# Optimization experiments

Measured on AMD Instinct MI355X. Metric: run time of the kernel, lower is better.

The kernel has to match this reference:

```python
import jax, jax.numpy as jnp
import numpy as np

D_EMB = 256
SCALE = 0.02
B, T = 4, 4096
EPS = 1e-5


def layer_norm(x, w, b):
    m = jnp.mean(x, axis=-1, keepdims=True)
    v = jnp.mean((x - m) ** 2, axis=-1, keepdims=True)
    return (x - m) * jax.lax.rsqrt(v + EPS) * w + b


def setup_inputs() -> dict:
    key = jax.random.key(0)
    ks = jax.random.split(key, 4)
    x = jax.random.normal(ks[0], (B, T, D_EMB), dtype=jnp.float32)
    qkv = jax.random.normal(ks[1], (3, D_EMB, D_EMB), dtype=jnp.float32) * SCALE
    # nn.Linear(D, 2D, bias=False): weight shape (2D, D), applied as x @ W.T
    w1 = jax.random.normal(ks[2], (2 * D_EMB, D_EMB), dtype=jnp.float32) * (1.0 / np.sqrt(D_EMB))
    w2 = jax.random.normal(ks[3], (D_EMB, 2 * D_EMB), dtype=jnp.float32) * (1.0 / np.sqrt(2 * D_EMB))
    ones = jnp.ones((D_EMB,), dtype=jnp.float32)
    zeros = jnp.zeros((D_EMB,), dtype=jnp.float32)
    return {
        "x": x, "qkv": qkv,
        "ln_q_w": ones, "ln_q_b": zeros,
        "ln_k_w": ones, "ln_k_b": zeros,
        "ln_attn_w": ones, "ln_attn_b": zeros,
        "w1": w1, "w2": w2,
        "ln_ff_w": ones, "ln_ff_b": zeros,
    }


def reference(x, qkv, ln_q_w, ln_q_b, ln_k_w, ln_k_b, ln_attn_w, ln_attn_b, w1, w2, ln_ff_w, ln_ff_b):
    # QKV projections: [3, B, T, D]
    y = jnp.einsum('btd,ndD->nbtD', x, qkv)
    q, k, v = y[0], y[1], y[2]
    q = layer_norm(q, ln_q_w, ln_q_b)
    k = layer_norm(k, ln_k_w, ln_k_b)
    # full (non-causal) single-head attention, scale by sqrt(D_EMB)
    scores = jnp.einsum('btd,bsd->bts', q, k) / jnp.sqrt(jnp.float32(D_EMB))
    attn = jax.nn.softmax(scores, axis=-1)
    y = jnp.einsum('bts,bsd->btd', attn, v)
    y = layer_norm(y, ln_attn_w, ln_attn_b)
    x = 0.7 * (x + y)
    # FFN with dual leaky_relu
    y = jax.nn.leaky_relu(x @ w1.T, negative_slope=0.2)
    y = jax.nn.leaky_relu(y @ w2.T, negative_slope=0.2)
    y = layer_norm(y, ln_ff_w, ln_ff_b)
    return 0.7 * (x + y)
```

## Files before the change

### kernel.cpp

```cpp
#include <hip/hip_runtime.h>

#define BSZ   4
#define TSEQ  4096
#define DEMB  256
#define NTOK  (BSZ * TSEQ)
#define HID   512
#define SPLITS 4
#define KEYS_PER_SPLIT (TSEQ / SPLITS)
#define TK 32
#define KIMG_STRIDE 8704
#define VIMG_STRIDE 10240

using bf16x8 = __attribute__((ext_vector_type(8))) short;
using f32x16 = __attribute__((ext_vector_type(16))) float;

static __device__ __forceinline__ unsigned short f2bf(float f) {
  union { float f; unsigned u; } v; v.f = f;
  unsigned r = v.u + 0x7FFF + ((v.u >> 16) & 1);
  return (unsigned short)(r >> 16);
}
static __device__ __forceinline__ float bf2f(unsigned short u) {
  union { unsigned u; float f; } v; v.u = ((unsigned)u) << 16;
  return v.f;
}

static __device__ __forceinline__ void async16(void* lds, const void* gp) {
  __builtin_amdgcn_global_load_lds(
      (const __attribute__((address_space(1))) unsigned int*)gp,
      (__attribute__((address_space(3))) unsigned int*)lds, 16, 0, 0);
}

__global__ __launch_bounds__(256) void qkvT_kernel(
    const float* __restrict__ qkv, unsigned short* __restrict__ qkvT)
{
  __shared__ float Ts[64][65];
  const int tid = threadIdx.x;
  const int k0 = blockIdx.x * 64;
  const int j0 = blockIdx.y * 64;
  const int z  = blockIdx.z;
  const float* src = qkv + (size_t)z * DEMB * DEMB + (size_t)k0 * DEMB + j0;
#pragma unroll
  for (int p = 0; p < 4; ++p) {
    int idx = p * 256 + tid;
    int r = idx >> 4, g = idx & 15;
    float4 v = *(const float4*)(src + (size_t)r * DEMB + g * 4);
    Ts[r][g * 4 + 0] = v.x; Ts[r][g * 4 + 1] = v.y;
    Ts[r][g * 4 + 2] = v.z; Ts[r][g * 4 + 3] = v.w;
  }
  __syncthreads();
  unsigned short* dst = qkvT + (size_t)z * DEMB * DEMB + (size_t)j0 * DEMB + k0;
#pragma unroll
  for (int p = 0; p < 4; ++p) {
    int idx = p * 256 + tid;
    int r = idx >> 4, g = idx & 15;
    ushort4 o;
    o.x = f2bf(Ts[g * 4 + 0][r]); o.y = f2bf(Ts[g * 4 + 1][r]);
    o.z = f2bf(Ts[g * 4 + 2][r]); o.w = f2bf(Ts[g * 4 + 3][r]);
    *(ushort4*)(dst + (size_t)r * DEMB + g * 4) = o;
  }
}

__global__ __launch_bounds__(256) void castw_kernel(
    const float* __restrict__ w1, const float* __restrict__ w2,
    unsigned short* __restrict__ w1b, unsigned short* __restrict__ w2b)
{
  const int i = blockIdx.x * 256 + threadIdx.x;
  const float* s = blockIdx.y ? w2 : w1;
  unsigned short* d = blockIdx.y ? w2b : w1b;
  float4 v = ((const float4*)s)[i];
  ushort4 o;
  o.x = f2bf(v.x); o.y = f2bf(v.y); o.z = f2bf(v.z); o.w = f2bf(v.w);
  ((ushort4*)d)[i] = o;
}

template <int ACT, int MODE, int AF32>
__global__ __launch_bounds__(256, 3) void gemm_bf16_kernel(
    const void* __restrict__ Av, const unsigned short* __restrict__ Bt,
    float* __restrict__ Cf, unsigned short* __restrict__ C0,
    unsigned short* __restrict__ C1, unsigned short* __restrict__ C2,
    int M, int N, int K)
{
  __shared__ __align__(16) unsigned short As[128 * 72];
  __shared__ __align__(16) unsigned short Bs[128 * 72];

  const int tid = threadIdx.x;
  const int w   = tid >> 6;
  const int wm  = w >> 1, wn = w & 1;
  const int l   = tid & 63;
  const int lm  = l & 31;
  const int lh  = l >> 5;

  const int m0    = blockIdx.x * 128;
  const int nbase = blockIdx.y * 128;

  f32x16 acc00, acc01, acc10, acc11;
#pragma unroll
  for (int r = 0; r < 16; ++r) { acc00[r] = 0.f; acc01[r] = 0.f; acc10[r] = 0.f; acc11[r] = 0.f; }

  const int lr = tid >> 3;
  const int lc = (tid & 7) * 8;
  const int fr = tid >> 4;
  const int fc = (tid & 15) * 4;

  const unsigned short* Ab = (const unsigned short*)Av;
  const float* Af = (const float*)Av;

  bf16x8 arb[4], brb[4];
  float4 arf[8];

#pragma unroll
  for (int i = 0; i < (AF32 ? 8 : 4); ++i) {
    if (AF32) arf[i] = *(const float4*)(Af + (size_t)(m0 + i * 16 + fr) * K + fc);
    else      arb[i] = *(const bf16x8*)(Ab + (size_t)(m0 + i * 32 + lr) * K + lc);
  }
#pragma unroll
  for (int i = 0; i < 4; ++i)
    brb[i] = *(const bf16x8*)(Bt + (size_t)(nbase + i * 32 + lr) * K + lc);

  for (int k0 = 0; k0 < K; k0 += 64) {
    __syncthreads();
    if (AF32) {
#pragma unroll
      for (int i = 0; i < 8; ++i) {
        ushort4 u;
        u.x = f2bf(arf[i].x); u.y = f2bf(arf[i].y);
        u.z = f2bf(arf[i].z); u.w = f2bf(arf[i].w);
        *(ushort4*)&As[(i * 16 + fr) * 72 + fc] = u;
      }
    } else {
#pragma unroll
      for (int i = 0; i < 4; ++i) *(bf16x8*)&As[(i * 32 + lr) * 72 + lc] = arb[i];
    }
#pragma unroll
    for (int i = 0; i < 4; ++i) *(bf16x8*)&Bs[(i * 32 + lr) * 72 + lc] = brb[i];
    __syncthreads();

    if (k0 + 64 < K) {
      const int kn = k0 + 64;
#pragma unroll
      for (int i = 0; i < (AF32 ? 8 : 4); ++i) {
        if (AF32) arf[i] = *(const float4*)(Af + (size_t)(m0 + i * 16 + fr) * K + kn + fc);
        else      arb[i] = *(const bf16x8*)(Ab + (size_t)(m0 + i * 32 + lr) * K + kn + lc);
      }
#pragma unroll
      for (int i = 0; i < 4; ++i)
        brb[i] = *(const bf16x8*)(Bt + (size_t)(nbase + i * 32 + lr) * K + kn + lc);
    }

#pragma unroll
    for (int ks = 0; ks < 4; ++ks) {
      bf16x8 a0 = *(const bf16x8*)&As[(wm * 64 + lm)      * 72 + ks * 16 + lh * 8];
      bf16x8 a1 = *(const bf16x8*)&As[(wm * 64 + 32 + lm) * 72 + ks * 16 + lh * 8];
      bf16x8 b0 = *(const bf16x8*)&Bs[(wn * 64 + lm)      * 72 + ks * 16 + lh * 8];
      bf16x8 b1 = *(const bf16x8*)&Bs[(wn * 64 + 32 + lm) * 72 + ks * 16 + lh * 8];
      acc00 = __builtin_amdgcn_mfma_f32_32x32x16_bf16(a0, b0, acc00, 0, 0, 0);
      acc01 = __builtin_amdgcn_mfma_f32_32x32x16_bf16(a0, b1, acc01, 0, 0, 0);
      acc10 = __builtin_amdgcn_mfma_f32_32x32x16_bf16(a1, b0, acc10, 0, 0, 0);
      acc11 = __builtin_amdgcn_mfma_f32_32x32x16_bf16(a1, b1, acc11, 0, 0, 0);
    }
  }

  unsigned short* Cb = C0;
  int col0, ldc;
  if (MODE == 2) {
    const int sel = blockIdx.y >> 1;
    Cb = (sel == 0) ? C0 : (sel == 1 ? C1 : C2);
    col0 = (blockIdx.y & 1) * 128;
    ldc = DEMB;
  } else {
    col0 = nbase;
    ldc = N;
  }
  const f32x16* accs[4] = { &acc00, &acc01, &acc10, &acc11 };
#pragma unroll
  for (int am = 0; am < 2; ++am)
#pragma unroll
    for (int bn = 0; bn < 2; ++bn) {
      const f32x16& a = *accs[am * 2 + bn];
#pragma unroll
      for (int r = 0; r < 16; ++r) {
        const int m = m0 + wm * 64 + am * 32 + (r & 3) + 8 * (r >> 2) + 4 * lh;
        const int n = col0 + wn * 64 + bn * 32 + lm;
        float v = a[r];
        if (ACT == 1) v = v > 0.f ? v : 0.2f * v;
        if (MODE == 0) Cf[(size_t)m * ldc + n] = v;
        else           Cb[(size_t)m * ldc + n] = f2bf(v);
      }
    }
}

template <int IMG>
__global__ __launch_bounds__(256) void ln_bf16b_kernel(
    const unsigned short* __restrict__ X, const float* __restrict__ w,
    const float* __restrict__ b, unsigned short* __restrict__ out)
{
  const int lane = threadIdx.x & 63;
  const size_t row = (size_t)blockIdx.x * 4 + (threadIdx.x >> 6);
  ushort4 u = *(const ushort4*)&X[row * DEMB + lane * 4];
  float x0 = bf2f(u.x), x1 = bf2f(u.y), x2 = bf2f(u.z), x3 = bf2f(u.w);
  float s  = x0 + x1 + x2 + x3;
  float sq = x0 * x0 + x1 * x1 + x2 * x2 + x3 * x3;
#pragma unroll
  for (int o = 32; o > 0; o >>= 1) { s += __shfl_down(s, o); sq += __shfl_down(sq, o); }
  s = __shfl(s, 0); sq = __shfl(sq, 0);
  const float m  = s * (1.f / DEMB);
  const float rs = rsqrtf(sq * (1.f / DEMB) - m * m + 1e-5f);
  const float4 wv = *(const float4*)&w[lane * 4];
  const float4 bv = *(const float4*)&b[lane * 4];
  ushort4 o;
  o.x = f2bf((x0 - m) * rs * wv.x + bv.x);
  o.y = f2bf((x1 - m) * rs * wv.y + bv.y);
  o.z = f2bf((x2 - m) * rs * wv.z + bv.z);
  o.w = f2bf((x3 - m) * rs * wv.w + bv.w);
  if (IMG == 0) {
    *(ushort4*)&out[row * DEMB + lane * 4] = o;
  } else {
    const int bb = (int)(row >> 12);
    const int t  = (int)(row & 4095);
    *(ushort4*)&out[(size_t)(bb * 128 + (t >> 5)) * KIMG_STRIDE + (t & 31) * 264 + lane * 4] = o;
  }
}

__global__ __launch_bounds__(256) void ln_res_kernel(
    const float* __restrict__ Y, const float* __restrict__ Xin,
    const float* __restrict__ w, const float* __restrict__ b,
    float* __restrict__ Out)
{
  const int lane = threadIdx.x & 63;
  const size_t row = (size_t)blockIdx.x * 4 + (threadIdx.x >> 6);
  float4 y = *(const float4*)&Y[row * DEMB + lane * 4];
  float s  = y.x + y.y + y.z + y.w;
  float sq = y.x * y.x + y.y * y.y + y.z * y.z + y.w * y.w;
#pragma unroll
  for (int o = 32; o > 0; o >>= 1) { s += __shfl_down(s, o); sq += __shfl_down(sq, o); }
  s = __shfl(s, 0); sq = __shfl(sq, 0);
  const float m  = s * (1.f / DEMB);
  const float rs = rsqrtf(sq * (1.f / DEMB) - m * m + 1e-5f);
  const float4 wv = *(const float4*)&w[lane * 4];
  const float4 bv = *(const float4*)&b[lane * 4];
  const float4 xi = *(const float4*)&Xin[row * DEMB + lane * 4];
  float4 o;
  o.x = 0.7f * (xi.x + (y.x - m) * rs * wv.x + bv.x);
  o.y = 0.7f * (xi.y + (y.y - m) * rs * wv.y + bv.y);
  o.z = 0.7f * (xi.z + (y.z - m) * rs * wv.z + bv.z);
  o.w = 0.7f * (xi.w + (y.w - m) * rs * wv.w + bv.w);
  *(float4*)&Out[row * DEMB + lane * 4] = o;
}

__global__ __launch_bounds__(256) void vtrans_img_kernel(
    const unsigned short* __restrict__ Vraw, unsigned short* __restrict__ Vimg)
{
  __shared__ float Ts[64][65];
  const int tid = threadIdx.x;
  const int t0 = blockIdx.x * 64;
  const int d0 = blockIdx.y * 64;
  const int b  = blockIdx.z;
  const unsigned short* src = Vraw + ((size_t)b * TSEQ + t0) * DEMB + d0;
#pragma unroll
  for (int p = 0; p < 4; ++p) {
    int idx = p * 256 + tid;
    int r = idx >> 4, g = idx & 15;
    ushort4 u = *(const ushort4*)(src + (size_t)r * DEMB + g * 4);
    Ts[r][g * 4 + 0] = bf2f(u.x); Ts[r][g * 4 + 1] = bf2f(u.y);
    Ts[r][g * 4 + 2] = bf2f(u.z); Ts[r][g * 4 + 3] = bf2f(u.w);
  }
  __syncthreads();
#pragma unroll
  for (int p = 0; p < 4; ++p) {
    int idx = p * 256 + tid;
    int r = idx >> 4, g = idx & 15;
    const int t  = t0 + g * 4;
    const int kt = t >> 5, toff = t & 31;
    ushort4 o;
    o.x = f2bf(Ts[g * 4 + 0][r]); o.y = f2bf(Ts[g * 4 + 1][r]);
    o.z = f2bf(Ts[g * 4 + 2][r]); o.w = f2bf(Ts[g * 4 + 3][r]);
    *(ushort4*)(Vimg + (size_t)(b * 128 + kt) * VIMG_STRIDE + (d0 + r) * 40 + toff) = o;
  }
}

__global__ __launch_bounds__(256, 2) void attn_split_kernel(
    const unsigned short* __restrict__ Qb, const unsigned short* __restrict__ Kimg,
    const unsigned short* __restrict__ Vimg, unsigned short* __restrict__ Opart,
    float* __restrict__ lpart)
{
  __shared__ __align__(16) unsigned short Ks[KIMG_STRIDE];
  __shared__ __align__(16) unsigned short Vs[2][VIMG_STRIDE];
  __shared__ __align__(16) unsigned short Pb[4 * 32 * 40];

  const int tid = threadIdx.x;
  const int w   = tid >> 6;
  const int l   = tid & 63;
  const int lm  = l & 31;
  const int lh  = l >> 5;

  const int lin = blockIdx.x;
  const int xcd = lin & 7;
  const int idx = lin >> 3;
  const int b     = xcd >> 1;
  const int split = (xcd & 1) * 2 + (idx & 1);
  const int q0    = (idx >> 1) * 128;

  const unsigned short* Qbase  = Qb + (size_t)b * TSEQ * DEMB;
  const unsigned short* Ktiles = Kimg + (size_t)(b * 128 + split * 32) * KIMG_STRIDE;
  const unsigned short* Vtiles = Vimg + (size_t)(b * 128 + split * 32) * VIMG_STRIDE;

  bf16x8 qf[16];
  {
    const unsigned short* qrow = Qbase + (size_t)(q0 + w * 32 + lm) * DEMB + lh * 8;
#pragma unroll
    for (int ks = 0; ks < 16; ++ks) qf[ks] = *(const bf16x8*)(qrow + ks * 16);
  }

  f32x16 o[8];
  float lsum[16];
#pragma unroll
  for (int t = 0; t < 8; ++t)
#pragma unroll
    for (int r = 0; r < 16; ++r) o[t][r] = 0.f;
#pragma unroll
  for (int r = 0; r < 16; ++r) lsum[r] = 0.f;

  unsigned short* Pw = &Pb[w * 32 * 40];

#pragma unroll
  for (int i = 0; i < 5; ++i) {
    const int c = w + i * 4;
    if (c < 17) async16(&Ks[c * 512], Ktiles + c * 512 + l * 8);
  }
#pragma unroll
  for (int i = 0; i < 5; ++i) {
    const int c = w * 5 + i;
    async16(&Vs[0][c * 512], Vtiles + c * 512 + l * 8);
  }

  for (int st = 0; st < KEYS_PER_SPLIT / TK; ++st) {
    __syncthreads();

    f32x16 sa, sb;
#pragma unroll
    for (int r = 0; r < 16; ++r) { sa[r] = 0.f; sb[r] = 0.f; }
#pragma unroll
    for (int ks = 0; ks < 8; ++ks) {
      bf16x8 kfa = *(const bf16x8*)&Ks[lm * 264 + (2 * ks)     * 16 + lh * 8];
      bf16x8 kfb = *(const bf16x8*)&Ks[lm * 264 + (2 * ks + 1) * 16 + lh * 8];
      sa = __builtin_amdgcn_mfma_f32_32x32x16_bf16(qf[2 * ks],     kfa, sa, 0, 0, 0);
      sb = __builtin_amdgcn_mfma_f32_32x32x16_bf16(qf[2 * ks + 1], kfb, sb, 0, 0, 0);
    }
    __syncthreads();

    const int nx = st + 1;
    if (nx < KEYS_PER_SPLIT / TK) {
#pragma unroll
      for (int i = 0; i < 5; ++i) {
        const int c = w + i * 4;
        if (c < 17) async16(&Ks[c * 512], Ktiles + (size_t)nx * KIMG_STRIDE + c * 512 + l * 8);
      }
    }

#pragma unroll
    for (int r = 0; r < 16; ++r) {
      const float p = exp2f((sa[r] + sb[r]) * 0.09016844335f - 11.541560327f);
      lsum[r] += p;
      const int row = (r & 3) + ((r >> 2) << 3) + (lh << 2);
      Pw[row * 40 + lm] = f2bf(p);
    }

    if (nx < KEYS_PER_SPLIT / TK) {
#pragma unroll
      for (int i = 0; i < 5; ++i) {
        const int c = w * 5 + i;
        async16(&Vs[nx & 1][c * 512], Vtiles + (size_t)nx * VIMG_STRIDE + c * 512 + l * 8);
      }
    }

#pragma unroll
    for (int ks = 0; ks < 2; ++ks) {
      bf16x8 pf = *(const bf16x8*)&Pw[lm * 40 + ks * 16 + lh * 8];
#pragma unroll
      for (int t = 0; t < 8; ++t) {
        bf16x8 vf = *(const bf16x8*)&Vs[st & 1][(t * 32 + lm) * 40 + ks * 16 + lh * 8];
        o[t] = __builtin_amdgcn_mfma_f32_32x32x16_bf16(pf, vf, o[t], 0, 0, 0);
      }
    }
  }

#pragma unroll
  for (int r = 0; r < 16; ++r) {
#pragma unroll
    for (int d = 1; d < 32; d <<= 1) lsum[r] += __shfl_xor(lsum[r], d, 64);
  }
  unsigned short* Ob =
      Opart + ((size_t)split * NTOK + (size_t)b * TSEQ + q0 + w * 32) * DEMB;
  float* lb = lpart + (size_t)split * NTOK + (size_t)b * TSEQ + q0 + w * 32;
#pragma unroll
  for (int r = 0; r < 16; ++r) {
    const int row = (r & 3) + ((r >> 2) << 3) + (lh << 2);
#pragma unroll
    for (int t = 0; t < 8; ++t)
      Ob[(size_t)row * DEMB + t * 32 + lm] = f2bf(o[t][r]);
    if (lm == 0) lb[row] = lsum[r];
  }
}

__global__ __launch_bounds__(256) void combine_lnres_kernel(
    const unsigned short* __restrict__ Opart, const float* __restrict__ lpart,
    const float* __restrict__ Xin, const float* __restrict__ w,
    const float* __restrict__ b, float* __restrict__ Out,
    unsigned short* __restrict__ Outb)
{
  const int lane = threadIdx.x & 63;
  const size_t row = (size_t)blockIdx.x * 4 + (threadIdx.x >> 6);
  float4 acc = make_float4(0.f, 0.f, 0.f, 0.f);
  float lt = 0.f;
#pragma unroll
  for (int p = 0; p < SPLITS; ++p) {
    const ushort4 u = *(const ushort4*)&Opart[((size_t)p * NTOK + row) * DEMB + lane * 4];
    acc.x += bf2f(u.x); acc.y += bf2f(u.y);
    acc.z += bf2f(u.z); acc.w += bf2f(u.w);
    lt += lpart[(size_t)p * NTOK + row];
  }
  const float inv = 1.f / lt;
  const float y0 = acc.x * inv, y1 = acc.y * inv, y2 = acc.z * inv, y3 = acc.w * inv;
  float s  = y0 + y1 + y2 + y3;
  float sq = y0 * y0 + y1 * y1 + y2 * y2 + y3 * y3;
#pragma unroll
  for (int o = 32; o > 0; o >>= 1) { s += __shfl_down(s, o); sq += __shfl_down(sq, o); }
  s = __shfl(s, 0); sq = __shfl(sq, 0);
  const float m  = s * (1.f / DEMB);
  const float rs = rsqrtf(sq * (1.f / DEMB) - m * m + 1e-5f);
  const float4 wv = *(const float4*)&w[lane * 4];
  const float4 bv = *(const float4*)&b[lane * 4];
  const float4 xi = *(const float4*)&Xin[row * DEMB + lane * 4];
  float4 o;
  o.x = 0.7f * (xi.x + (y0 - m) * rs * wv.x + bv.x);
  o.y = 0.7f * (xi.y + (y1 - m) * rs * wv.y + bv.y);
  o.z = 0.7f * (xi.z + (y2 - m) * rs * wv.z + bv.z);
  o.w = 0.7f * (xi.w + (y3 - m) * rs * wv.w + bv.w);
  *(float4*)&Out[row * DEMB + lane * 4] = o;
  ushort4 ob;
  ob.x = f2bf(o.x); ob.y = f2bf(o.y); ob.z = f2bf(o.z); ob.w = f2bf(o.w);
  *(ushort4*)&Outb[row * DEMB + lane * 4] = ob;
}

extern "C" void kernel_launch(void* const* d_in, const int* in_sizes, int n_in,
                              void* d_out, int out_size, void* d_ws, size_t ws_size,
                              hipStream_t stream)
{
  (void)in_sizes; (void)n_in; (void)out_size; (void)ws_size;
  const float* x    = (const float*)d_in[0];
  const float* qkv  = (const float*)d_in[1];
  const float* lnqw = (const float*)d_in[2];
  const float* lnqb = (const float*)d_in[3];
  const float* lnkw = (const float*)d_in[4];
  const float* lnkb = (const float*)d_in[5];
  const float* lnaw = (const float*)d_in[6];
  const float* lnab = (const float*)d_in[7];
  const float* w1   = (const float*)d_in[8];
  const float* w2   = (const float*)d_in[9];
  const float* lnfw = (const float*)d_in[10];
  const float* lnfb = (const float*)d_in[11];
  float* out = (float*)d_out;

  char* W = (char*)d_ws;
  const size_t MB = 1 << 20;
  unsigned short* Qraw  = (unsigned short*)(W + 8 * MB);
  unsigned short* Kraw  = (unsigned short*)(W + 16 * MB);
  unsigned short* Vraw  = (unsigned short*)(W + 24 * MB);
  unsigned short* Qbn   = (unsigned short*)(W + 32 * MB);
  unsigned short* Kimg  = (unsigned short*)(W + 40 * MB);
  unsigned short* Vimg  = (unsigned short*)(W + 49 * MB);
  unsigned short* Opart = (unsigned short*)(W + 0);
  float*          lpart = (float*)(W + 61 * MB);
  unsigned short* x1b   = (unsigned short*)(W + 32 * MB);
  unsigned short* H     = (unsigned short*)(W + 40 * MB);
  float*          Y2    = (float*)(W + 0);
  unsigned short* qkvT  = (unsigned short*)(W + 60 * MB);
  unsigned short* w1b   = (unsigned short*)(W + 60 * MB + 512 * 1024);
  unsigned short* w2b   = (unsigned short*)(W + 60 * MB + 768 * 1024);

  const dim3 blk(256);

  qkvT_kernel<<<dim3(4, 4, 3), blk, 0, stream>>>(qkv, qkvT);
  castw_kernel<<<dim3(128, 2), blk, 0, stream>>>(w1, w2, w1b, w2b);

  gemm_bf16_kernel<0, 2, 1><<<dim3(NTOK / 128, 6), blk, 0, stream>>>(
      x, qkvT, nullptr, Qraw, Kraw, Vraw, NTOK, 3 * DEMB, DEMB);

  ln_bf16b_kernel<0><<<NTOK / 4, blk, 0, stream>>>(Qraw, lnqw, lnqb, Qbn);
  ln_bf16b_kernel<1><<<NTOK / 4, blk, 0, stream>>>(Kraw, lnkw, lnkb, Kimg);
  vtrans_img_kernel<<<dim3(TSEQ / 64, DEMB / 64, BSZ), blk, 0, stream>>>(Vraw, Vimg);

  attn_split_kernel<<<dim3(512), blk, 0, stream>>>(Qbn, Kimg, Vimg, Opart, lpart);
  combine_lnres_kernel<<<NTOK / 4, blk, 0, stream>>>(Opart, lpart, x, lnaw, lnab, out, x1b);

  gemm_bf16_kernel<1, 1, 0><<<dim3(NTOK / 128, HID / 128), blk, 0, stream>>>(
      x1b, w1b, nullptr, H, nullptr, nullptr, NTOK, HID, DEMB);
  gemm_bf16_kernel<1, 0, 0><<<dim3(NTOK / 128, DEMB / 128), blk, 0, stream>>>(
      H, w2b, Y2, nullptr, nullptr, nullptr, NTOK, DEMB, HID);

  ln_res_kernel<<<NTOK / 4, blk, 0, stream>>>(Y2, out, lnfw, lnfb, out);
}
```

Before: 263.8 us.

## Double-buffer K/V in 512-thread attention blocks and merge small prep/LN launches

The attention kernel now runs 8 waves per block over 256 queries, so K/V tiles loaded into LDS are shared by twice as many query rows. K is now double-buffered like V, with a single barrier per step and the next tile prefetched before the QK MFMAs. Separately, the weight transpose/cast kernels are merged into one launch and the Q/K layer norms into one launch, cutting launch count. The larger block uses more LDS (two K buffers) and halves the grid to 256 blocks, which may reduce occupancy and latency hiding.

```diff
diff --git a/kernel.cpp b/kernel.cpp
--- a/kernel.cpp
+++ b/kernel.cpp
@@ -30,47 +30,47 @@
       (__attribute__((address_space(3))) unsigned int*)lds, 16, 0, 0);
 }
 
-__global__ __launch_bounds__(256) void qkvT_kernel(
-    const float* __restrict__ qkv, unsigned short* __restrict__ qkvT)
-{
-  __shared__ float Ts[64][65];
+__global__ __launch_bounds__(256) void prep_kernel(
+    const float* __restrict__ qkv, const float* __restrict__ w1,
+    const float* __restrict__ w2, unsigned short* __restrict__ qkvT,
+    unsigned short* __restrict__ w1b, unsigned short* __restrict__ w2b)
+{
   const int tid = threadIdx.x;
-  const int k0 = blockIdx.x * 64;
-  const int j0 = blockIdx.y * 64;
-  const int z  = blockIdx.z;
-  const float* src = qkv + (size_t)z * DEMB * DEMB + (size_t)k0 * DEMB + j0;
-#pragma unroll
-  for (int p = 0; p < 4; ++p) {
-    int idx = p * 256 + tid;
-    int r = idx >> 4, g = idx & 15;
-    float4 v = *(const float4*)(src + (size_t)r * DEMB + g * 4);
-    Ts[r][g * 4 + 0] = v.x; Ts[r][g * 4 + 1] = v.y;
-    Ts[r][g * 4 + 2] = v.z; Ts[r][g * 4 + 3] = v.w;
-  }
-  __syncthreads();
-  unsigned short* dst = qkvT + (size_t)z * DEMB * DEMB + (size_t)j0 * DEMB + k0;
-#pragma unroll
-  for (int p = 0; p < 4; ++p) {
-    int idx = p * 256 + tid;
-    int r = idx >> 4, g = idx & 15;
+  if (blockIdx.y < 3) {
+    if (blockIdx.x >= 16) return;
+    __shared__ float Ts[64][65];
+    const int z  = blockIdx.y;
+    const int k0 = (blockIdx.x >> 2) * 64;
+    const int j0 = (blockIdx.x & 3) * 64;
+    const float* src = qkv + (size_t)z * DEMB * DEMB + (size_t)k0 * DEMB + j0;
+#pragma unroll
+    for (int p = 0; p < 4; ++p) {
+      int idx = p * 256 + tid;
+      int r = idx >> 4, g = idx & 15;
+      float4 v = *(const float4*)(src + (size_t)r * DEMB + g * 4);
+      Ts[r][g * 4 + 0] = v.x; Ts[r][g * 4 + 1] = v.y;
+      Ts[r][g * 4 + 2] = v.z; Ts[r][g * 4 + 3] = v.w;
+    }
+    __syncthreads();
+    unsigned short* dst = qkvT + (size_t)z * DEMB * DEMB + (size_t)j0 * DEMB + k0;
+#pragma unroll
+    for (int p = 0; p < 4; ++p) {
+      int idx = p * 256 + tid;
+      int r = idx >> 4, g = idx & 15;
+      ushort4 o;
+      o.x = f2bf(Ts[g * 4 + 0][r]); o.y = f2bf(Ts[g * 4 + 1][r]);
+      o.z = f2bf(Ts[g * 4 + 2][r]); o.w = f2bf(Ts[g * 4 + 3][r]);
+      *(ushort4*)(dst + (size_t)r * DEMB + g * 4) = o;
+    }
+  } else {
+    const float* s = (blockIdx.y == 3) ? w1 : w2;
+    unsigned short* d = (blockIdx.y == 3) ? w1b : w2b;
+    const int i = blockIdx.x * 256 + tid;
+    float4 v = ((const float4*)s)[i];
     ushort4 o;
-    o.x = f2bf(Ts[g * 4 + 0][r]); o.y = f2bf(Ts[g * 4 + 1][r]);
-    o.z = f2bf(Ts[g * 4 + 2][r]); o.w = f2bf(Ts[g * 4 + 3][r]);
-    *(ushort4*)(dst + (size_t)r * DEMB + g * 4) = o;
-  }
-}
-
-__global__ __launch_bounds__(256) void castw_kernel(
-    const float* __restrict__ w1, const float* __restrict__ w2,
-    unsigned short* __restrict__ w1b, unsigned short* __restrict__ w2b)
-{
-  const int i = blockIdx.x * 256 + threadIdx.x;
-  const float* s = blockIdx.y ? w2 : w1;
-  unsigned short* d = blockIdx.y ? w2b : w1b;
-  float4 v = ((const float4*)s)[i];
-  ushort4 o;
-  o.x = f2bf(v.x); o.y = f2bf(v.y); o.z = f2bf(v.z); o.w = f2bf(v.w);
-  ((ushort4*)d)[i] = o;
+    o.x = f2bf(v.x); o.y = f2bf(v.y); o.z = f2bf(v.z); o.w = f2bf(v.w);
+    ((ushort4*)d)[i] = o;
+  }
 }
 
 template <int ACT, int MODE, int AF32>
@@ -189,11 +189,16 @@
     }
 }
 
-template <int IMG>
-__global__ __launch_bounds__(256) void ln_bf16b_kernel(
-    const unsigned short* __restrict__ X, const float* __restrict__ w,
-    const float* __restrict__ b, unsigned short* __restrict__ out)
-{
+__global__ __launch_bounds__(256) void ln_qk_kernel(
+    const unsigned short* __restrict__ Qraw, const unsigned short* __restrict__ Kraw,
+    const float* __restrict__ qw, const float* __restrict__ qb,
+    const float* __restrict__ kw, const float* __restrict__ kb,
+    unsigned short* __restrict__ Qbn, unsigned short* __restrict__ Kimg)
+{
+  const int isK = blockIdx.y;
+  const unsigned short* X = isK ? Kraw : Qraw;
+  const float* w = isK ? kw : qw;
+  const float* b = isK ? kb : qb;
   const int lane = threadIdx.x & 63;
   const size_t row = (size_t)blockIdx.x * 4 + (threadIdx.x >> 6);
   ushort4 u = *(const ushort4*)&X[row * DEMB + lane * 4];
@@ -212,12 +217,12 @@
   o.y = f2bf((x1 - m) * rs * wv.y + bv.y);
   o.z = f2bf((x2 - m) * rs * wv.z + bv.z);
   o.w = f2bf((x3 - m) * rs * wv.w + bv.w);
-  if (IMG == 0) {
-    *(ushort4*)&out[row * DEMB + lane * 4] = o;
+  if (!isK) {
+    *(ushort4*)&Qbn[row * DEMB + lane * 4] = o;
   } else {
     const int bb = (int)(row >> 12);
     const int t  = (int)(row & 4095);
-    *(ushort4*)&out[(size_t)(bb * 128 + (t >> 5)) * KIMG_STRIDE + (t & 31) * 264 + lane * 4] = o;
+    *(ushort4*)&Kimg[(size_t)(bb * 128 + (t >> 5)) * KIMG_STRIDE + (t & 31) * 264 + lane * 4] = o;
   }
 }
 
@@ -278,14 +283,14 @@
   }
 }
 
-__global__ __launch_bounds__(256, 2) void attn_split_kernel(
+__global__ __launch_bounds__(512) void attn_split_kernel(
     const unsigned short* __restrict__ Qb, const unsigned short* __restrict__ Kimg,
     const unsigned short* __restrict__ Vimg, unsigned short* __restrict__ Opart,
     float* __restrict__ lpart)
 {
-  __shared__ __align__(16) unsigned short Ks[KIMG_STRIDE];
+  __shared__ __align__(16) unsigned short Ks[2][KIMG_STRIDE];
   __shared__ __align__(16) unsigned short Vs[2][VIMG_STRIDE];
-  __shared__ __align__(16) unsigned short Pb[4 * 32 * 40];
+  __shared__ __align__(16) unsigned short Pb[8 * 32 * 40];
 
   const int tid = threadIdx.x;
   const int w   = tid >> 6;
@@ -298,7 +303,7 @@
   const int idx = lin >> 3;
   const int b     = xcd >> 1;
   const int split = (xcd & 1) * 2 + (idx & 1);
-  const int q0    = (idx >> 1) * 128;
+  const int q0    = (idx >> 1) * 256;
 
   const unsigned short* Qbase  = Qb + (size_t)b * TSEQ * DEMB;
   const unsigned short* Ktiles = Kimg + (size_t)(b * 128 + split * 32) * KIMG_STRIDE;
@@ -323,54 +328,52 @@
   unsigned short* Pw = &Pb[w * 32 * 40];
 
 #pragma unroll
-  for (int i = 0; i < 5; ++i) {
-    const int c = w + i * 4;
-    if (c < 17) async16(&Ks[c * 512], Ktiles + c * 512 + l * 8);
-  }
-#pragma unroll
-  for (int i = 0; i < 5; ++i) {
-    const int c = w * 5 + i;
-    async16(&Vs[0][c * 512], Vtiles + c * 512 + l * 8);
+  for (int i = 0; i < 3; ++i) {
+    const int c = w + 8 * i;
+    if (c < 17) async16(&Ks[0][c * 512], Ktiles + c * 512 + l * 8);
+  }
+#pragma unroll
+  for (int i = 0; i < 3; ++i) {
+    const int c = w + 8 * i;
+    if (c < 20) async16(&Vs[0][c * 512], Vtiles + c * 512 + l * 8);
   }
 
   for (int st = 0; st < KEYS_PER_SPLIT / TK; ++st) {
+    const int p = st & 1;
     __syncthreads();
 
+    if (st + 1 < KEYS_PER_SPLIT / TK) {
+      const unsigned short* kn = Ktiles + (size_t)(st + 1) * KIMG_STRIDE;
+      const unsigned short* vn = Vtiles + (size_t)(st + 1) * VIMG_STRIDE;
+#pragma unroll
+      for (int i = 0; i < 3; ++i) {
+        const int c = w + 8 * i;
+        if (c < 17) async16(&Ks[1 - p][c * 512], kn + c * 512 + l * 8);
+      }
+#pragma unroll
+      for (int i = 0; i < 3; ++i) {
+        const int c = w + 8 * i;
+        if (c < 20) async16(&Vs[1 - p][c * 512], vn + c * 512 + l * 8);
+      }
+    }
+
     f32x16 sa, sb;
 #pragma unroll
     for (int r = 0; r < 16; ++r) { sa[r] = 0.f; sb[r] = 0.f; }
 #pragma unroll
     for (int ks = 0; ks < 8; ++ks) {
-      bf16x8 kfa = *(const bf16x8*)&Ks[lm * 264 + (2 * ks)     * 16 + lh * 8];
-      bf16x8 kfb = *(const bf16x8*)&Ks[lm * 264 + (2 * ks + 1) * 16 + lh * 8];
+      bf16x8 kfa = *(const bf16x8*)&Ks[p][lm * 264 + (2 * ks)     * 16 + lh * 8];
+      bf16x8 kfb = *(const bf16x8*)&Ks[p][lm * 264 + (2 * ks + 1) * 16 + lh * 8];
       sa = __builtin_amdgcn_mfma_f32_32x32x16_bf16(qf[2 * ks],     kfa, sa, 0, 0, 0);
       sb = __builtin_amdgcn_mfma_f32_32x32x16_bf16(qf[2 * ks + 1], kfb, sb, 0, 0, 0);
     }
-    __syncthreads();
-
-    const int nx = st + 1;
-    if (nx < KEYS_PER_SPLIT / TK) {
-#pragma unroll
-      for (int i = 0; i < 5; ++i) {
-        const int c = w + i * 4;
-        if (c < 17) async16(&Ks[c * 512], Ktiles + (size_t)nx * KIMG_STRIDE + c * 512 + l * 8);
-      }
-    }
 
 #pragma unroll
     for (int r = 0; r < 16; ++r) {
-      const float p = exp2f((sa[r] + sb[r]) * 0.09016844335f - 11.541560327f);
-      lsum[r] += p;
+      const float pv = exp2f((sa[r] + sb[r]) * 0.09016844335f - 11.541560327f);
+      lsum[r] += pv;
       const int row = (r & 3) + ((r >> 2) << 3) + (lh << 2);
-      Pw[row * 40 + lm] = f2bf(p);
-    }
-
-    if (nx < KEYS_PER_SPLIT / TK) {
-#pragma unroll
-      for (int i = 0; i < 5; ++i) {
-        const int c = w * 5 + i;
-        async16(&Vs[nx & 1][c * 512], Vtiles + (size_t)nx * VIMG_STRIDE + c * 512 + l * 8);
-      }
+      Pw[row * 40 + lm] = f2bf(pv);
     }
 
 #pragma unroll
@@ -378,7 +381,7 @@
       bf16x8 pf = *(const bf16x8*)&Pw[lm * 40 + ks * 16 + lh * 8];
 #pragma unroll
       for (int t = 0; t < 8; ++t) {
-        bf16x8 vf = *(const bf16x8*)&Vs[st & 1][(t * 32 + lm) * 40 + ks * 16 + lh * 8];
+        bf16x8 vf = *(const bf16x8*)&Vs[p][(t * 32 + lm) * 40 + ks * 16 + lh * 8];
         o[t] = __builtin_amdgcn_mfma_f32_32x32x16_bf16(pf, vf, o[t], 0, 0, 0);
       }
     }
@@ -480,17 +483,16 @@
 
   const dim3 blk(256);
 
-  qkvT_kernel<<<dim3(4, 4, 3), blk, 0, stream>>>(qkv, qkvT);
-  castw_kernel<<<dim3(128, 2), blk, 0, stream>>>(w1, w2, w1b, w2b);
+  prep_kernel<<<dim3(128, 5), blk, 0, stream>>>(qkv, w1, w2, qkvT, w1b, w2b);
 
   gemm_bf16_kernel<0, 2, 1><<<dim3(NTOK / 128, 6), blk, 0, stream>>>(
       x, qkvT, nullptr, Qraw, Kraw, Vraw, NTOK, 3 * DEMB, DEMB);
 
-  ln_bf16b_kernel<0><<<NTOK / 4, blk, 0, stream>>>(Qraw, lnqw, lnqb, Qbn);
-  ln_bf16b_kernel<1><<<NTOK / 4, blk, 0, stream>>>(Kraw, lnkw, lnkb, Kimg);
+  ln_qk_kernel<<<dim3(NTOK / 4, 2), blk, 0, stream>>>(
+      Qraw, Kraw, lnqw, lnqb, lnkw, lnkb, Qbn, Kimg);
   vtrans_img_kernel<<<dim3(TSEQ / 64, DEMB / 64, BSZ), blk, 0, stream>>>(Vraw, Vimg);
 
-  attn_split_kernel<<<dim3(512), blk, 0, stream>>>(Qbn, Kimg, Vimg, Opart, lpart);
+  attn_split_kernel<<<dim3(256), dim3(512), 0, stream>>>(Qbn, Kimg, Vimg, Opart, lpart);
   combine_lnres_kernel<<<NTOK / 4, blk, 0, stream>>>(Opart, lpart, x, lnaw, lnab, out, x1b);
 
   gemm_bf16_kernel<1, 1, 0><<<dim3(NTOK / 128, HID / 128), blk, 0, stream>>>(
```

Result: faster. 255.0 us (-3.3%).
